# Kernel tuning notes

Measured on AMD Instinct MI355X. Metric: run time of the kernel, lower is better.

Reference implementation:

```python
import jax, jax.numpy as jnp
import numpy as np

K_NEAREST = 5
EPS = 1e-6


def setup_inputs() -> dict:
    key = jax.random.key(0)
    k1, k2, k3 = jax.random.split(key, 3)
    N_Q, N_DB, D_OUT, D_AUX = 4096, 65536, 32, 32
    return {
        "embedding_features": jax.random.normal(k1, (N_Q, D_OUT), dtype=jnp.float32),
        "db_embedding": jax.random.normal(k2, (N_DB, D_OUT), dtype=jnp.float32),
        "auxiliary_features": jax.random.normal(k3, (N_DB, D_AUX), dtype=jnp.float32),
    }


def reference(embedding_features, db_embedding, auxiliary_features):
    d_out = embedding_features.shape[-1]
    q = embedding_features.reshape(-1, d_out)          # [Nq, D]
    db = db_embedding.reshape(-1, d_out)               # [Ndb, D]

    # Euclidean cdist via the expanded quadratic form (same math as torch.cdist p=2).
    q_sq = jnp.sum(q * q, axis=1, keepdims=True)       # [Nq, 1]
    db_sq = jnp.sum(db * db, axis=1)[None, :]          # [1, Ndb]
    dist_sq = q_sq + db_sq - 2.0 * (q @ db.T)          # [Nq, Ndb]
    distances = jnp.sqrt(jnp.maximum(dist_sq, 0.0))

    # k smallest distances == k largest of negated distances.
    neg_top, nearest_indices = jax.lax.top_k(-distances, K_NEAREST)  # [Nq, k]
    nearest_distances = -neg_top                                      # [Nq, k]

    aux = auxiliary_features.reshape(-1, auxiliary_features.shape[-1])
    nearest_aux = aux[nearest_indices]                 # [Nq, k, Daux]

    weights = 1.0 / (nearest_distances + EPS)
    weights = weights / jnp.sum(weights, axis=1, keepdims=True)

    return jnp.sum(nearest_aux * weights[..., None], axis=1)  # [Nq, Daux]
```

## Files before the change

### kernel.cpp

```cpp
#include <hip/hip_runtime.h>
#include <math.h>

#define N_Q   4096
#define N_DB  65536
#define DIM   32
#define KNN   5
#define NC    64
#define CH    (N_DB / NC)
#define TS    128
#define NSTG  (CH / TS)
#define NSUB  (TS / 32)
#define NCAND (NC * 6)
#define BIAS  256.0f

typedef _Float16 half8  __attribute__((ext_vector_type(8)));
typedef __fp16   fp16x2 __attribute__((ext_vector_type(2)));
typedef float floatx16  __attribute__((ext_vector_type(16)));

union H8  { half8 h; uint4 u4; unsigned u[4]; };
union F16 { floatx16 v; float4 q4[4]; unsigned w[16]; };
union HU  { fp16x2 h2; unsigned u; };

__device__ __forceinline__ unsigned cvt2(float a, float b) {
    HU t; t.h2 = __builtin_amdgcn_cvt_pkrtz(a, b);
    return t.u;
}

__device__ __forceinline__ void ld_lds16(const void* g, void* l) {
    __builtin_amdgcn_global_load_lds((const __attribute__((address_space(1))) unsigned*)g,
                                     (__attribute__((address_space(3))) unsigned*)l, 16, 0, 0);
}
__device__ __forceinline__ void ld_lds4(const void* g, void* l) {
    __builtin_amdgcn_global_load_lds((const __attribute__((address_space(1))) unsigned*)g,
                                     (__attribute__((address_space(3))) unsigned*)l, 4, 0, 0);
}

__global__ __launch_bounds__(256) void k_prep(const float* __restrict__ DB,
                                              uint4* __restrict__ DBh,
                                              float* __restrict__ hdb) {
    int p = blockIdx.x * 256 + threadIdx.x;
    const float4* src = (const float4*)(DB + (size_t)p * DIM);
    float4 f[8]; float s = 0.f;
#pragma unroll
    for (int j = 0; j < 8; ++j) {
        f[j] = src[j];
        s += f[j].x * f[j].x + f[j].y * f[j].y + f[j].z * f[j].z + f[j].w * f[j].w;
    }
    hdb[p] = BIAS - 0.5f * s;
    int t = p >> 5, r = p & 31;
#pragma unroll
    for (int gi = 0; gi < 4; ++gi) {
        uint4 g;
        g.x = cvt2(f[2 * gi].x, f[2 * gi].y);
        g.y = cvt2(f[2 * gi].z, f[2 * gi].w);
        g.z = cvt2(f[2 * gi + 1].x, f[2 * gi + 1].y);
        g.w = cvt2(f[2 * gi + 1].z, f[2 * gi + 1].w);
        DBh[(size_t)t * 128 + gi * 32 + r] = g;
    }
}

__global__ __launch_bounds__(256, 6) void k_scan(const float* __restrict__ Q,
                                                 const uint4* __restrict__ DBh,
                                                 const float* __restrict__ hdb,
                                                 unsigned* __restrict__ cand) {
    __shared__ char  dbs[2][8192];
    __shared__ float hbs[2][TS];

    const int tid = threadIdx.x, lane = tid & 63, w = tid >> 6;
    const int h = lane >> 5, qcol = lane & 31;
    const int chunk = blockIdx.x & (NC - 1);
    const int qb    = blockIdx.x >> 6;
    const int q     = qb * 128 + w * 32 + qcol;
    const int pbase = chunk * CH;

    const float* qp = Q + (size_t)q * DIM;
    float4 qa = *(const float4*)(qp + h * 8);
    float4 qb4 = *(const float4*)(qp + h * 8 + 4);
    float4 qc = *(const float4*)(qp + 16 + h * 8);
    float4 qd = *(const float4*)(qp + 16 + h * 8 + 4);
    H8 b1, b2;
    b1.u[0] = cvt2(qa.x, qa.y);   b1.u[1] = cvt2(qa.z, qa.w);
    b1.u[2] = cvt2(qb4.x, qb4.y); b1.u[3] = cvt2(qb4.z, qb4.w);
    b2.u[0] = cvt2(qc.x, qc.y);   b2.u[1] = cvt2(qc.z, qc.w);
    b2.u[2] = cvt2(qd.x, qd.y);   b2.u[3] = cvt2(qd.z, qd.w);

    unsigned maskv;
    asm("v_mov_b32 %0, 0xFFFFFC00" : "=v"(maskv));

    auto stage = [&](int buf, int t) {
        const char* s = (const char*)DBh + (size_t)pbase * 64 + (size_t)t * 8192
                        + w * 1024 + lane * 16;
        char* d = dbs[buf] + w * 1024;
        ld_lds16(s, d);
        ld_lds16(s + 4096, d + 4096);
        if (w < 2)
            ld_lds4(hdb + pbase + t * TS + w * 64 + lane,
                    (char*)&hbs[buf][0] + w * 256);
    };

    float tk[6];
#pragma unroll
    for (int r = 0; r < 6; ++r) tk[r] = 0.f;

    constexpr int ROWC[16] = {0,1,2,3, 8,9,10,11, 16,17,18,19, 24,25,26,27};

    stage(0, 0);
    for (int t = 0; t < NSTG; ++t) {
        __syncthreads();
        if (t + 1 < NSTG) stage((t + 1) & 1, t + 1);
        const int buf = t & 1;
        const char* base = dbs[buf];
#pragma unroll
        for (int sub = 0; sub < NSUB; ++sub) {
            const char* tb = base + sub * 2048;
            H8 a1, a2;
            a1.u4 = *(const uint4*)(tb + h * 512 + (lane & 31) * 16);
            a2.u4 = *(const uint4*)(tb + 1024 + h * 512 + (lane & 31) * 16);
            F16 c0;
            const float* hb = &hbs[buf][sub * 32 + 4 * h];
            c0.q4[0] = *(const float4*)(hb + 0);
            c0.q4[1] = *(const float4*)(hb + 8);
            c0.q4[2] = *(const float4*)(hb + 16);
            c0.q4[3] = *(const float4*)(hb + 24);
            floatx16 acc = __builtin_amdgcn_mfma_f32_32x32x16_f16(a1.h, b1.h, c0.v, 0, 0, 0);
            acc = __builtin_amdgcn_mfma_f32_32x32x16_f16(a2.h, b2.h, acc, 0, 0, 0);
            F16 pk; pk.v = acc;
            const int meta = (t * NSUB + sub) << 5;
            float p[16];
#pragma unroll
            for (int r = 0; r < 16; ++r)
                p[r] = __uint_as_float((pk.w[r] & maskv) | (unsigned)(meta | ROWC[r]));
            float hi[8], lo[8];
#pragma unroll
            for (int i = 0; i < 8; ++i) { hi[i] = fmaxf(p[2*i], p[2*i+1]); lo[i] = fminf(p[2*i], p[2*i+1]); }
            float H4[4], L4[4];
#pragma unroll
            for (int i = 0; i < 4; ++i) {
                H4[i] = fmaxf(hi[2*i], hi[2*i+1]);
                L4[i] = fmaxf(fmaxf(lo[2*i], lo[2*i+1]), fminf(hi[2*i], hi[2*i+1]));
            }
            float H2[2], L2[2];
#pragma unroll
            for (int i = 0; i < 2; ++i) {
                H2[i] = fmaxf(H4[2*i], H4[2*i+1]);
                L2[i] = fmaxf(fmaxf(L4[2*i], L4[2*i+1]), fminf(H4[2*i], H4[2*i+1]));
            }
            float c1 = fmaxf(H2[0], H2[1]);
            float c2 = fmaxf(fmaxf(L2[0], L2[1]), fminf(H2[0], H2[1]));
            {
                float m01 = fminf(tk[0], c1), m02 = fminf(tk[1], c1);
                float m03 = fminf(tk[2], c1), m04 = fminf(tk[3], c1);
                float m05 = fminf(tk[4], c1);
                float m12 = fminf(tk[0], c2), m13 = fminf(tk[1], c2);
                float m14 = fminf(tk[2], c2), m15 = fminf(tk[3], c2);
                tk[0] = fmaxf(tk[0], c1);
                tk[1] = fmaxf(fmaxf(tk[1], m01), c2);
                tk[2] = fmaxf(fmaxf(tk[2], m02), m12);
                tk[3] = fmaxf(fmaxf(tk[3], m03), m13);
                tk[4] = fmaxf(fmaxf(tk[4], m04), m14);
                tk[5] = fmaxf(fmaxf(tk[5], m05), m15);
            }
        }
    }

#pragma unroll
    for (int r = 0; r < 6; ++r)
        tk[r] = __uint_as_float(__float_as_uint(tk[r]) | (unsigned)(h << 2));

    float other[6];
#pragma unroll
    for (int i = 0; i < 6; ++i) other[i] = __shfl_xor(tk[i], 32, 64);
#pragma unroll
    for (int i = 0; i < 6; ++i) {
        float val = other[i];
#pragma unroll
        for (int j = 0; j < 6; ++j) { float mx = fmaxf(tk[j], val); val = fminf(tk[j], val); tk[j] = mx; }
    }
    if (h == 0) {
        unsigned* dst = cand + ((size_t)q * NC + chunk) * 6;
#pragma unroll
        for (int r = 0; r < 6; ++r) dst[r] = __float_as_uint(tk[r]);
    }
}

__global__ __launch_bounds__(256) void k_merge(const float* __restrict__ Q,
                                               const float* __restrict__ DB,
                                               const float* __restrict__ AUX,
                                               const unsigned* __restrict__ cand,
                                               float* __restrict__ out) {
    const int tid = threadIdx.x, lane = tid & 63, w = tid >> 6;
    const int q = blockIdx.x * 4 + w;

    const unsigned* cq = cand + (size_t)q * NCAND + (size_t)lane * 6;
    float cur[6];
#pragma unroll
    for (int r = 0; r < 6; ++r) cur[r] = __uint_as_float(cq[r]);

    float wv[12]; int wl[12];
#pragma unroll
    for (int r = 0; r < 12; ++r) {
        float bv = cur[0]; int bl = lane;
#pragma unroll
        for (int off = 32; off >= 1; off >>= 1) {
            float ov = __shfl_xor(bv, off, 64);
            int   ol = __shfl_xor(bl, off, 64);
            if (ov > bv || (ov == bv && ol < bl)) { bv = ov; bl = ol; }
        }
        wv[r] = bv; wl[r] = bl;
        if (bl == lane) {
#pragma unroll
            for (int s = 0; s < 5; ++s) cur[s] = cur[s + 1];
            cur[5] = -1.f;
        }
    }

    float dist = 1e30f; int dbi = 0x7fffffff;
    if (lane < 12) {
        unsigned u = __float_as_uint(wv[lane]) & 1023u;
        dbi = wl[lane] * CH + (int)u;
        const float4* dp = (const float4*)(DB + (size_t)dbi * DIM);
        const float4* qp = (const float4*)(Q + (size_t)q * DIM);
        float dot = 0.f, qs = 0.f, ds = 0.f;
#pragma unroll
        for (int j = 0; j < DIM / 4; ++j) {
            float4 a = qp[j], d = dp[j];
            dot += a.x * d.x + a.y * d.y + a.z * d.z + a.w * d.w;
            qs  += a.x * a.x + a.y * a.y + a.z * a.z + a.w * a.w;
            ds  += d.x * d.x + d.y * d.y + d.z * d.z + d.w * d.w;
        }
        dist = sqrtf(fmaxf(qs + ds - 2.f * dot, 0.f));
    }
    float wd[KNN]; int wi[KNN];
#pragma unroll
    for (int r = 0; r < KNN; ++r) {
        float bd = dist; int bi = dbi;
#pragma unroll
        for (int off = 32; off >= 1; off >>= 1) {
            float od = __shfl_xor(bd, off, 64);
            int   oi = __shfl_xor(bi, off, 64);
            if (od < bd || (od == bd && oi < bi)) { bd = od; bi = oi; }
        }
        wd[r] = bd; wi[r] = bi;
        if (dist == bd && dbi == bi) dist = 1e30f;
    }
    float ww[KNN], W = 0.f;
#pragma unroll
    for (int r = 0; r < KNN; ++r) { ww[r] = 1.f / (wd[r] + 1e-6f); W += ww[r]; }
    if (lane < DIM) {
        float o = 0.f;
#pragma unroll
        for (int r = 0; r < KNN; ++r) o += ww[r] * AUX[(size_t)wi[r] * DIM + lane];
        out[(size_t)q * DIM + lane] = o / W;
    }
}

extern "C" void kernel_launch(void* const* d_in, const int* in_sizes, int n_in,
                              void* d_out, int out_size, void* d_ws, size_t ws_size,
                              hipStream_t stream) {
    const float* Q   = (const float*)d_in[0];
    const float* DB  = (const float*)d_in[1];
    const float* AUX = (const float*)d_in[2];
    float* out = (float*)d_out;

    char* ws = (char*)d_ws;
    uint4*    DBh = (uint4*)ws;                         ws += (size_t)(N_DB / 32) * 128 * 16;
    float*    hdb = (float*)ws;                         ws += (size_t)N_DB * 4;
    unsigned* cand = (unsigned*)ws;

    k_prep<<<N_DB / 256, 256, 0, stream>>>(DB, DBh, hdb);
    k_scan<<<(N_Q / 128) * NC, 256, 0, stream>>>(Q, DBh, hdb, cand);
    k_merge<<<N_Q / 4, 256, 0, stream>>>(Q, DB, AUX, cand, out);
}
```

Before: 137.6 us.

## Load DB tiles directly from global into registers instead of LDS staging

```diff
diff --git a/kernel.cpp b/kernel.cpp
--- a/kernel.cpp
+++ b/kernel.cpp
@@ -7,9 +7,7 @@
 #define KNN   5
 #define NC    64
 #define CH    (N_DB / NC)
-#define TS    128
-#define NSTG  (CH / TS)
-#define NSUB  (TS / 32)
+#define NSUB  32
 #define NCAND (NC * 6)
 #define BIAS  256.0f
 
@@ -24,15 +22,6 @@
 __device__ __forceinline__ unsigned cvt2(float a, float b) {
     HU t; t.h2 = __builtin_amdgcn_cvt_pkrtz(a, b);
     return t.u;
-}
-
-__device__ __forceinline__ void ld_lds16(const void* g, void* l) {
-    __builtin_amdgcn_global_load_lds((const __attribute__((address_space(1))) unsigned*)g,
-                                     (__attribute__((address_space(3))) unsigned*)l, 16, 0, 0);
-}
-__device__ __forceinline__ void ld_lds4(const void* g, void* l) {
-    __builtin_amdgcn_global_load_lds((const __attribute__((address_space(1))) unsigned*)g,
-                                     (__attribute__((address_space(3))) unsigned*)l, 4, 0, 0);
 }
 
 __global__ __launch_bounds__(256) void k_prep(const float* __restrict__ DB,
@@ -63,9 +52,6 @@
                                                  const uint4* __restrict__ DBh,
                                                  const float* __restrict__ hdb,
                                                  unsigned* __restrict__ cand) {
-    __shared__ char  dbs[2][8192];
-    __shared__ float hbs[2][TS];
-
     const int tid = threadIdx.x, lane = tid & 63, w = tid >> 6;
     const int h = lane >> 5, qcol = lane & 31;
     const int chunk = blockIdx.x & (NC - 1);
@@ -87,80 +73,74 @@
     unsigned maskv;
     asm("v_mov_b32 %0, 0xFFFFFC00" : "=v"(maskv));
 
-    auto stage = [&](int buf, int t) {
-        const char* s = (const char*)DBh + (size_t)pbase * 64 + (size_t)t * 8192
-                        + w * 1024 + lane * 16;
-        char* d = dbs[buf] + w * 1024;
-        ld_lds16(s, d);
-        ld_lds16(s + 4096, d + 4096);
-        if (w < 2)
-            ld_lds4(hdb + pbase + t * TS + w * 64 + lane,
-                    (char*)&hbs[buf][0] + w * 256);
+    const uint4* abase = DBh + (size_t)(pbase >> 5) * 128 + h * 32 + (lane & 31);
+    const float* hb0   = hdb + pbase + 4 * h;
+
+    float tk[6];
+#pragma unroll
+    for (int r = 0; r < 6; ++r) tk[r] = 0.f;
+
+    constexpr int ROWC[16] = {0,1,2,3, 8,9,10,11, 16,17,18,19, 24,25,26,27};
+
+    auto compute = [&](const H8& A1, const H8& A2, const int s) {
+        const float* hbp = hb0 + s * 32;
+        F16 c0;
+        c0.q4[0] = *(const float4*)(hbp + 0);
+        c0.q4[1] = *(const float4*)(hbp + 8);
+        c0.q4[2] = *(const float4*)(hbp + 16);
+        c0.q4[3] = *(const float4*)(hbp + 24);
+        floatx16 acc = __builtin_amdgcn_mfma_f32_32x32x16_f16(A1.h, b1.h, c0.v, 0, 0, 0);
+        acc = __builtin_amdgcn_mfma_f32_32x32x16_f16(A2.h, b2.h, acc, 0, 0, 0);
+        F16 pk; pk.v = acc;
+        const int meta = s << 5;
+        float p[16];
+#pragma unroll
+        for (int r = 0; r < 16; ++r)
+            p[r] = __uint_as_float((pk.w[r] & maskv) | (unsigned)(meta | ROWC[r]));
+        float hi[8], lo[8];
+#pragma unroll
+        for (int i = 0; i < 8; ++i) { hi[i] = fmaxf(p[2*i], p[2*i+1]); lo[i] = fminf(p[2*i], p[2*i+1]); }
+        float H4[4], L4[4];
+#pragma unroll
+        for (int i = 0; i < 4; ++i) {
+            H4[i] = fmaxf(hi[2*i], hi[2*i+1]);
+            L4[i] = fmaxf(fmaxf(lo[2*i], lo[2*i+1]), fminf(hi[2*i], hi[2*i+1]));
+        }
+        float H2[2], L2[2];
+#pragma unroll
+        for (int i = 0; i < 2; ++i) {
+            H2[i] = fmaxf(H4[2*i], H4[2*i+1]);
+            L2[i] = fmaxf(fmaxf(L4[2*i], L4[2*i+1]), fminf(H4[2*i], H4[2*i+1]));
+        }
+        float c1 = fmaxf(H2[0], H2[1]);
+        float c2 = fmaxf(fmaxf(L2[0], L2[1]), fminf(H2[0], H2[1]));
+        {
+            float m01 = fminf(tk[0], c1), m02 = fminf(tk[1], c1);
+            float m03 = fminf(tk[2], c1), m04 = fminf(tk[3], c1);
+            float m05 = fminf(tk[4], c1);
+            float m12 = fminf(tk[0], c2), m13 = fminf(tk[1], c2);
+            float m14 = fminf(tk[2], c2), m15 = fminf(tk[3], c2);
+            tk[0] = fmaxf(tk[0], c1);
+            tk[1] = fmaxf(fmaxf(tk[1], m01), c2);
+            tk[2] = fmaxf(fmaxf(tk[2], m02), m12);
+            tk[3] = fmaxf(fmaxf(tk[3], m03), m13);
+            tk[4] = fmaxf(fmaxf(tk[4], m04), m14);
+            tk[5] = fmaxf(fmaxf(tk[5], m05), m15);
+        }
     };
 
-    float tk[6];
-#pragma unroll
-    for (int r = 0; r < 6; ++r) tk[r] = 0.f;
-
-    constexpr int ROWC[16] = {0,1,2,3, 8,9,10,11, 16,17,18,19, 24,25,26,27};
-
-    stage(0, 0);
-    for (int t = 0; t < NSTG; ++t) {
-        __syncthreads();
-        if (t + 1 < NSTG) stage((t + 1) & 1, t + 1);
-        const int buf = t & 1;
-        const char* base = dbs[buf];
-#pragma unroll
-        for (int sub = 0; sub < NSUB; ++sub) {
-            const char* tb = base + sub * 2048;
-            H8 a1, a2;
-            a1.u4 = *(const uint4*)(tb + h * 512 + (lane & 31) * 16);
-            a2.u4 = *(const uint4*)(tb + 1024 + h * 512 + (lane & 31) * 16);
-            F16 c0;
-            const float* hb = &hbs[buf][sub * 32 + 4 * h];
-            c0.q4[0] = *(const float4*)(hb + 0);
-            c0.q4[1] = *(const float4*)(hb + 8);
-            c0.q4[2] = *(const float4*)(hb + 16);
-            c0.q4[3] = *(const float4*)(hb + 24);
-            floatx16 acc = __builtin_amdgcn_mfma_f32_32x32x16_f16(a1.h, b1.h, c0.v, 0, 0, 0);
-            acc = __builtin_amdgcn_mfma_f32_32x32x16_f16(a2.h, b2.h, acc, 0, 0, 0);
-            F16 pk; pk.v = acc;
-            const int meta = (t * NSUB + sub) << 5;
-            float p[16];
-#pragma unroll
-            for (int r = 0; r < 16; ++r)
-                p[r] = __uint_as_float((pk.w[r] & maskv) | (unsigned)(meta | ROWC[r]));
-            float hi[8], lo[8];
-#pragma unroll
-            for (int i = 0; i < 8; ++i) { hi[i] = fmaxf(p[2*i], p[2*i+1]); lo[i] = fminf(p[2*i], p[2*i+1]); }
-            float H4[4], L4[4];
-#pragma unroll
-            for (int i = 0; i < 4; ++i) {
-                H4[i] = fmaxf(hi[2*i], hi[2*i+1]);
-                L4[i] = fmaxf(fmaxf(lo[2*i], lo[2*i+1]), fminf(hi[2*i], hi[2*i+1]));
-            }
-            float H2[2], L2[2];
-#pragma unroll
-            for (int i = 0; i < 2; ++i) {
-                H2[i] = fmaxf(H4[2*i], H4[2*i+1]);
-                L2[i] = fmaxf(fmaxf(L4[2*i], L4[2*i+1]), fminf(H4[2*i], H4[2*i+1]));
-            }
-            float c1 = fmaxf(H2[0], H2[1]);
-            float c2 = fmaxf(fmaxf(L2[0], L2[1]), fminf(H2[0], H2[1]));
-            {
-                float m01 = fminf(tk[0], c1), m02 = fminf(tk[1], c1);
-                float m03 = fminf(tk[2], c1), m04 = fminf(tk[3], c1);
-                float m05 = fminf(tk[4], c1);
-                float m12 = fminf(tk[0], c2), m13 = fminf(tk[1], c2);
-                float m14 = fminf(tk[2], c2), m15 = fminf(tk[3], c2);
-                tk[0] = fmaxf(tk[0], c1);
-                tk[1] = fmaxf(fmaxf(tk[1], m01), c2);
-                tk[2] = fmaxf(fmaxf(tk[2], m02), m12);
-                tk[3] = fmaxf(fmaxf(tk[3], m03), m13);
-                tk[4] = fmaxf(fmaxf(tk[4], m04), m14);
-                tk[5] = fmaxf(fmaxf(tk[5], m05), m15);
-            }
-        }
+    H8 a1A, a2A, a1B, a2B;
+    a1A.u4 = abase[0];
+    a2A.u4 = abase[64];
+    for (int s = 0; s < NSUB; s += 2) {
+        a1B.u4 = abase[(size_t)(s + 1) * 128];
+        a2B.u4 = abase[(size_t)(s + 1) * 128 + 64];
+        compute(a1A, a2A, s);
+        if (s + 2 < NSUB) {
+            a1A.u4 = abase[(size_t)(s + 2) * 128];
+            a2A.u4 = abase[(size_t)(s + 2) * 128 + 64];
+        }
+        compute(a1B, a2B, s + 1);
     }
 
 #pragma unroll
```

Measured after the change: 143.0 us. 1.04x slower.
